# Kernel tuning notes

Hardware: AMD Instinct MI355X
Metric: run time of the kernel (lower is better)

Reference implementation:

```python
import jax, jax.numpy as jnp
import numpy as np


def _v2v_mean(X, pair_v, pair_e, num_edges):
    """Hypergraph v2v mean aggregation: vertex->edge mean, then edge->vertex mean.
    X: [N, C] vertex features; (pair_v, pair_e): incidence pairs."""
    num_v = X.shape[0]
    ones = jnp.ones((pair_v.shape[0],), X.dtype)
    # v2e mean: average member-vertex features per hyperedge
    e_sum = jax.ops.segment_sum(X[pair_v], pair_e, num_segments=num_edges)
    e_cnt = jax.ops.segment_sum(ones, pair_e, num_segments=num_edges)
    Xe = e_sum / jnp.maximum(e_cnt, 1.0)[:, None]  # [E, C]
    # e2v mean: average incident-hyperedge features per vertex
    v_sum = jax.ops.segment_sum(Xe[pair_e], pair_v, num_segments=num_v)
    v_cnt = jax.ops.segment_sum(ones, pair_v, num_segments=num_v)
    return v_sum / jnp.maximum(v_cnt, 1.0)[:, None]  # [N, C]


def setup_inputs() -> dict:
    key = jax.random.key(0)
    ks = jax.random.split(key, 6)
    N, E, P = 16384, 2048, 262144          # vertices, hyperedges, incidence pairs
    Cin, Ch, Cout = 1024, 1024, 512
    feature_hyg = jax.random.normal(ks[0], (N, Cin), jnp.float32)
    pair_v = jax.random.randint(ks[1], (P,), 0, N)
    pair_e = jax.random.randint(ks[2], (P,), 0, E)
    W1 = jax.random.normal(ks[3], (Cin, Ch), jnp.float32) / np.float32(np.sqrt(Cin))
    b1 = jnp.zeros((Ch,), jnp.float32)
    W2 = jax.random.normal(ks[4], (Ch, Cout), jnp.float32) / np.float32(np.sqrt(Ch))
    b2 = jnp.zeros((Cout,), jnp.float32)
    return {"feature_hyg": feature_hyg, "pair_v": pair_v, "pair_e": pair_e,
            "num_edges": E, "W1": W1, "b1": b1, "W2": W2, "b2": b2}


def reference(feature_hyg, pair_v, pair_e, num_edges, W1, b1, W2, b2):
    # HGNNPConv layer 1 (use_bn=False, drop_rate=0.0, eval-mode dropout)
    X = jax.nn.relu(feature_hyg @ W1 + b1)   # theta + relu
    X = _v2v_mean(X, pair_v, pair_e, num_edges)
    X = jax.nn.relu(X)                       # self.act (dropout is identity)
    # HGNNPConv layer 2 (is_last=True)
    X = jax.nn.relu(X @ W2 + b2)
    X = _v2v_mean(X, pair_v, pair_e, num_edges)
    return X
```

## Files before the change

### kernel.cpp

```cpp
#include <hip/hip_runtime.h>

typedef __attribute__((ext_vector_type(8))) short short8;
typedef __attribute__((ext_vector_type(4))) float f32x4;

constexpr int Nv   = 16384;
constexpr int Ne   = 2048;
constexpr int Np   = 262144;
constexpr int Cin  = 1024;
constexpr int Chid = 1024;
constexpr int Cout = 512;

__device__ __forceinline__ ushort f2bf(float f){
  unsigned u = __float_as_uint(f);
  u += 0x7FFFu + ((u >> 16) & 1u);
  return (ushort)(u >> 16);
}
__device__ __forceinline__ float bf2f(ushort h){
  return __uint_as_float(((unsigned)h) << 16);
}

__device__ __forceinline__ void gload16(const void* g, void* lds){
  __builtin_amdgcn_global_load_lds(
      (const __attribute__((address_space(1))) void*)g,
      (__attribute__((address_space(3))) void*)lds, 16, 0, 0);
}


__global__ void count_pairs(const int* __restrict__ pv, const int* __restrict__ pe,
                            int* __restrict__ vcnt, int* __restrict__ ecnt){
  int p = blockIdx.x * blockDim.x + threadIdx.x;
  if (p < Np){
    atomicAdd(&ecnt[pe[p]], 1);
    atomicAdd(&vcnt[pv[p]], 1);
  }
}

__global__ void scan_excl(const int* __restrict__ cnt, int* __restrict__ off, int n){
  __shared__ int wsum[16];
  __shared__ int carry_s;
  const int lane = threadIdx.x & 63, wid = threadIdx.x >> 6;
  if (threadIdx.x == 0) carry_s = 0;
  __syncthreads();
  for (int base = 0; base < n; base += 1024){
    int i = base + (int)threadIdx.x;
    int v = (i < n) ? cnt[i] : 0;
    int s = v;
#pragma unroll
    for (int d = 1; d < 64; d <<= 1){
      int t = __shfl_up(s, d, 64);
      if (lane >= d) s += t;
    }
    if (lane == 63) wsum[wid] = s;
    __syncthreads();
    int wadd = 0;
#pragma unroll
    for (int w = 0; w < 16; ++w) if (w < wid) wadd += wsum[w];
    int carry = carry_s;
    if (i < n) off[i] = carry + wadd + s - v;
    __syncthreads();
    if (threadIdx.x == 1023) carry_s = carry + wadd + s;
    __syncthreads();
  }
  if (threadIdx.x == 0) off[n] = carry_s;
}

__global__ void fill_adj(const int* __restrict__ pv, const int* __restrict__ pe,
                         const int* __restrict__ eoff, int* __restrict__ efill, int* __restrict__ eadj,
                         const int* __restrict__ voff, int* __restrict__ vfill, int* __restrict__ vadj){
  int p = blockIdx.x * blockDim.x + threadIdx.x;
  if (p < Np){
    int e = pe[p], v = pv[p];
    int ie = atomicAdd(&efill[e], 1);
    eadj[eoff[e] + ie] = v;
    int iv = atomicAdd(&vfill[v], 1);
    vadj[voff[v] + iv] = e;
  }
}


__global__ void cvt_f32_bf16(const float* __restrict__ in, ushort* __restrict__ out, int n4){
  int i = blockIdx.x * blockDim.x + threadIdx.x;
  if (i < n4){
    float4 f = ((const float4*)in)[i];
    ushort4 o;
    o.x = f2bf(f.x); o.y = f2bf(f.y); o.z = f2bf(f.z); o.w = f2bf(f.w);
    ((ushort4*)out)[i] = o;
  }
}

__global__ void transpose_cvt(const float* __restrict__ in, ushort* __restrict__ out,
                              int R, int Ccols){
  __shared__ float t[32][33];
  int c0 = blockIdx.x * 32, r0 = blockIdx.y * 32;
  int tx = threadIdx.x, ty = threadIdx.y;
  for (int j = 0; j < 32; j += 8)
    t[ty + j][tx] = in[(size_t)(r0 + ty + j) * Ccols + (c0 + tx)];
  __syncthreads();
  for (int j = 0; j < 32; j += 8)
    out[(size_t)(c0 + ty + j) * R + (r0 + tx)] = f2bf(t[tx][ty + j]);
}


template<bool BIAS_RELU, bool OUT_BF16>
__global__ __launch_bounds__(256) void gemm_bt(
    const ushort* __restrict__ A, const ushort* __restrict__ BT,
    const float* __restrict__ bias, void* __restrict__ out,
    int M, int Nn, int K)
{
  __shared__ ushort As[128 * 32];
  __shared__ ushort Bs[128 * 32];
  const int tid  = threadIdx.x;
  const int lane = tid & 63;
  const int wave = tid >> 6;
  const int wm = wave >> 1, wn = wave & 1;
  const int m0 = blockIdx.x * 128, n0 = blockIdx.y * 128;

  f32x4 acc[4][4] = {};

  const int srow = tid >> 2;
  const int scol = (tid & 3) * 8;
  ushort* ldsA0 = &As[(wave * 16) * 32];
  ushort* ldsA1 = &As[(64 + wave * 16) * 32];
  ushort* ldsB0 = &Bs[(wave * 16) * 32];
  ushort* ldsB1 = &Bs[(64 + wave * 16) * 32];

  const int fr = lane & 15;
  const int kb = (lane >> 4) * 8;

  const size_t arow0 = (size_t)(m0 + srow) * K;
  const size_t arow1 = (size_t)(m0 + 64 + srow) * K;
  const size_t brow0 = (size_t)(n0 + srow) * K;
  const size_t brow1 = (size_t)(n0 + 64 + srow) * K;

  for (int k0 = 0; k0 < K; k0 += 32){
    __syncthreads();
    gload16(A  + arow0 + k0 + scol, ldsA0);
    gload16(A  + arow1 + k0 + scol, ldsA1);
    gload16(BT + brow0 + k0 + scol, ldsB0);
    gload16(BT + brow1 + k0 + scol, ldsB1);
    __syncthreads();

    short8 af[4], bfv[4];
#pragma unroll
    for (int m = 0; m < 4; ++m) af[m]  = *(const short8*)&As[(wm * 64 + m * 16 + fr) * 32 + kb];
#pragma unroll
    for (int n = 0; n < 4; ++n) bfv[n] = *(const short8*)&Bs[(wn * 64 + n * 16 + fr) * 32 + kb];
#pragma unroll
    for (int m = 0; m < 4; ++m)
#pragma unroll
      for (int n = 0; n < 4; ++n)
        acc[m][n] = __builtin_amdgcn_mfma_f32_16x16x32_bf16(af[m], bfv[n], acc[m][n], 0, 0, 0);
  }

#pragma unroll
  for (int m = 0; m < 4; ++m){
#pragma unroll
    for (int n = 0; n < 4; ++n){
      int row0 = m0 + wm * 64 + m * 16 + ((lane >> 4) * 4);
      int col  = n0 + wn * 64 + n * 16 + (lane & 15);
      float bv = BIAS_RELU ? bias[col] : 0.0f;
#pragma unroll
      for (int i = 0; i < 4; ++i){
        int row = row0 + i;
        float v = acc[m][n][i];
        if (BIAS_RELU){ v += bv; v = v > 0.0f ? v : 0.0f; }
        if (OUT_BF16) ((ushort*)out)[(size_t)row * Nn + col] = f2bf(v);
        else          ((float*) out)[(size_t)row * Nn + col] = v;
      }
    }
  }
}


template<bool BIASRELU, bool OUTBF16>
__global__ void seg_mean512(const ushort* __restrict__ Xin, const int* __restrict__ off,
                            const int* __restrict__ adj, const float* __restrict__ bias,
                            void* __restrict__ out){
  __shared__ int idx[128];
  const int s = blockIdx.x;
  const int tid = threadIdx.x;
  const int c = tid * 4;
  const int beg = off[s], end = off[s + 1];
  float a0 = 0.f, a1 = 0.f, a2 = 0.f, a3 = 0.f;
  for (int base = beg; base < end; base += 128){
    int nch = min(128, end - base);
    __syncthreads();
    if (tid < nch) idx[tid] = adj[base + tid];
    __syncthreads();
#pragma unroll 4
    for (int j = 0; j < nch; ++j){
      const ushort4 x = *(const ushort4*)&Xin[(size_t)idx[j] * 512 + c];
      a0 += bf2f(x.x); a1 += bf2f(x.y); a2 += bf2f(x.z); a3 += bf2f(x.w);
    }
  }
  float inv = 1.0f / (float)max(end - beg, 1);
  a0 *= inv; a1 *= inv; a2 *= inv; a3 *= inv;
  if (BIASRELU){
    const float4 b = *(const float4*)&bias[c];
    a0 = fmaxf(a0 + b.x, 0.f); a1 = fmaxf(a1 + b.y, 0.f);
    a2 = fmaxf(a2 + b.z, 0.f); a3 = fmaxf(a3 + b.w, 0.f);
  }
  if (OUTBF16){
    ushort4 o = {f2bf(a0), f2bf(a1), f2bf(a2), f2bf(a3)};
    *(ushort4*)&((ushort*)out)[(size_t)s * 512 + c] = o;
  } else {
    float4 o = {a0, a1, a2, a3};
    *(float4*)&((float*)out)[(size_t)s * 512 + c] = o;
  }
}


extern "C" void kernel_launch(void* const* d_in, const int* in_sizes, int n_in,
                              void* d_out, int out_size, void* d_ws, size_t ws_size,
                              hipStream_t stream){
  (void)in_sizes; (void)n_in; (void)out_size; (void)ws_size;
  const float* feat = (const float*)d_in[0];
  const int*   pv   = (const int*)d_in[1];
  const int*   pe   = (const int*)d_in[2];
  const float* W1   = (const float*)d_in[4];
  const float* b1   = (const float*)d_in[5];
  const float* W2   = (const float*)d_in[6];
  const float* b2   = (const float*)d_in[7];

  char* ws = (char*)d_ws;
  size_t off = 0;
  auto alloc = [&](size_t bytes) -> void* {
    void* p = ws + off;
    off += (bytes + 255) & ~(size_t)255;
    return p;
  };

  char* buf0 = (char*)alloc((size_t)Nv * Cin * 2);
  ushort* Abf = (ushort*)buf0;
  ushort* Y1  = (ushort*)buf0;
  ushort* X3  = (ushort*)(buf0 + (size_t)Nv * Cout * 2);
  ushort* X1bf = (ushort*)alloc((size_t)Nv * Chid * 2);
  ushort* Ze   = (ushort*)alloc((size_t)Ne * Cout * 2);
  ushort* Xe2  = (ushort*)alloc((size_t)Ne * Cout * 2);
  ushort* W1T  = (ushort*)alloc((size_t)Chid * Cin * 2);
  ushort* W2T  = (ushort*)alloc((size_t)Cout * Chid * 2);

  int* zr     = (int*)alloc((size_t)(Ne + Nv + Ne + Nv) * 4);
  int* e_cnt  = zr;
  int* v_cnt  = zr + Ne;
  int* e_fill = zr + Ne + Nv;
  int* v_fill = zr + Ne + Nv + Ne;
  int* e_off  = (int*)alloc((size_t)(Ne + 1) * 4);
  int* v_off  = (int*)alloc((size_t)(Nv + 1) * 4);
  int* e_adj  = (int*)alloc((size_t)Np * 4);
  int* v_adj  = (int*)alloc((size_t)Np * 4);

  hipMemsetAsync(zr, 0, (size_t)(Ne + Nv + Ne + Nv) * 4, stream);
  count_pairs<<<(Np + 255) / 256, 256, 0, stream>>>(pv, pe, v_cnt, e_cnt);
  scan_excl<<<1, 1024, 0, stream>>>(e_cnt, e_off, Ne);
  scan_excl<<<1, 1024, 0, stream>>>(v_cnt, v_off, Nv);
  fill_adj<<<(Np + 255) / 256, 256, 0, stream>>>(pv, pe, e_off, e_fill, e_adj,
                                                 v_off, v_fill, v_adj);

  cvt_f32_bf16<<<(Nv * Cin / 4 + 255) / 256, 256, 0, stream>>>(feat, Abf, Nv * Cin / 4);
  transpose_cvt<<<dim3(Chid / 32, Cin / 32), dim3(32, 8), 0, stream>>>(W1, W1T, Cin, Chid);
  transpose_cvt<<<dim3(Cout / 32, Chid / 32), dim3(32, 8), 0, stream>>>(W2, W2T, Chid, Cout);

  gemm_bt<true, true><<<dim3(Nv / 128, Chid / 128), 256, 0, stream>>>(
      Abf, W1T, b1, X1bf, Nv, Chid, Cin);

  gemm_bt<false, true><<<dim3(Nv / 128, Cout / 128), 256, 0, stream>>>(
      X1bf, W2T, nullptr, Y1, Nv, Cout, Chid);

  seg_mean512<false, true><<<Ne, 128, 0, stream>>>(Y1, e_off, e_adj, nullptr, Ze);

  seg_mean512<true, true><<<Nv, 128, 0, stream>>>(Ze, v_off, v_adj, b2, X3);

  seg_mean512<false, true><<<Ne, 128, 0, stream>>>(X3, e_off, e_adj, nullptr, Xe2);
  seg_mean512<false, false><<<Nv, 128, 0, stream>>>(Xe2, v_off, v_adj, nullptr, (float*)d_out);
}
```

Measured before the change: 420.6 us.

## Double-buffer GEMM LDS tiles and split segment-mean rows across four waves

The GEMM now double-buffers its A/B LDS tiles, issuing the async global-to-LDS load for the next K-slice before running the MFMAs on the current one, with a single barrier per iteration. This is meant to hide load latency behind compute. The segment-mean kernel moves to 256 threads: each of four waves gathers a different subset of rows with 16-byte loads and two independent accumulators, then the partial sums are reduced through LDS. This raises memory-level parallelism for the gather, at the cost of extra LDS use and a reduction step.

```diff
diff --git a/kernel.cpp b/kernel.cpp
--- a/kernel.cpp
+++ b/kernel.cpp
@@ -107,8 +107,8 @@
     const float* __restrict__ bias, void* __restrict__ out,
     int M, int Nn, int K)
 {
-  __shared__ ushort As[128 * 32];
-  __shared__ ushort Bs[128 * 32];
+  __shared__ ushort As[2][128 * 32];
+  __shared__ ushort Bs[2][128 * 32];
   const int tid  = threadIdx.x;
   const int lane = tid & 63;
   const int wave = tid >> 6;
@@ -119,10 +119,8 @@
 
   const int srow = tid >> 2;
   const int scol = (tid & 3) * 8;
-  ushort* ldsA0 = &As[(wave * 16) * 32];
-  ushort* ldsA1 = &As[(64 + wave * 16) * 32];
-  ushort* ldsB0 = &Bs[(wave * 16) * 32];
-  ushort* ldsB1 = &Bs[(64 + wave * 16) * 32];
+  const int ldsbase0 = (wave * 16) * 32;
+  const int ldsbase1 = (64 + wave * 16) * 32;
 
   const int fr = lane & 15;
   const int kb = (lane >> 4) * 8;
@@ -132,24 +130,35 @@
   const size_t brow0 = (size_t)(n0 + srow) * K;
   const size_t brow1 = (size_t)(n0 + 64 + srow) * K;
 
-  for (int k0 = 0; k0 < K; k0 += 32){
-    __syncthreads();
-    gload16(A  + arow0 + k0 + scol, ldsA0);
-    gload16(A  + arow1 + k0 + scol, ldsA1);
-    gload16(BT + brow0 + k0 + scol, ldsB0);
-    gload16(BT + brow1 + k0 + scol, ldsB1);
-    __syncthreads();
+  const int nt = K >> 5;
+
+  auto stage = [&](int b, int k0){
+    gload16(A  + arow0 + k0 + scol, &As[b][ldsbase0]);
+    gload16(A  + arow1 + k0 + scol, &As[b][ldsbase1]);
+    gload16(BT + brow0 + k0 + scol, &Bs[b][ldsbase0]);
+    gload16(BT + brow1 + k0 + scol, &Bs[b][ldsbase1]);
+  };
+
+  stage(0, 0);
+  __syncthreads();
+
+  int cur = 0;
+  for (int t = 0; t < nt; ++t){
+    if (t + 1 < nt) stage(cur ^ 1, (t + 1) * 32);
 
     short8 af[4], bfv[4];
 #pragma unroll
-    for (int m = 0; m < 4; ++m) af[m]  = *(const short8*)&As[(wm * 64 + m * 16 + fr) * 32 + kb];
-#pragma unroll
-    for (int n = 0; n < 4; ++n) bfv[n] = *(const short8*)&Bs[(wn * 64 + n * 16 + fr) * 32 + kb];
+    for (int m = 0; m < 4; ++m) af[m]  = *(const short8*)&As[cur][(wm * 64 + m * 16 + fr) * 32 + kb];
+#pragma unroll
+    for (int n = 0; n < 4; ++n) bfv[n] = *(const short8*)&Bs[cur][(wn * 64 + n * 16 + fr) * 32 + kb];
 #pragma unroll
     for (int m = 0; m < 4; ++m)
 #pragma unroll
       for (int n = 0; n < 4; ++n)
         acc[m][n] = __builtin_amdgcn_mfma_f32_16x16x32_bf16(af[m], bfv[n], acc[m][n], 0, 0, 0);
+
+    __syncthreads();
+    cur ^= 1;
   }
 
 #pragma unroll
@@ -173,39 +182,63 @@
 
 
 template<bool BIASRELU, bool OUTBF16>
-__global__ void seg_mean512(const ushort* __restrict__ Xin, const int* __restrict__ off,
-                            const int* __restrict__ adj, const float* __restrict__ bias,
-                            void* __restrict__ out){
-  __shared__ int idx[128];
+__global__ __launch_bounds__(256) void seg_mean512(
+    const ushort* __restrict__ Xin, const int* __restrict__ off,
+    const int* __restrict__ adj, const float* __restrict__ bias,
+    void* __restrict__ out){
+  __shared__ int idx[256];
+  __shared__ float part[4][512];
   const int s = blockIdx.x;
-  const int tid = threadIdx.x;
-  const int c = tid * 4;
+  const int tid  = threadIdx.x;
+  const int lane = tid & 63;
+  const int wv   = tid >> 6;
+  const int c0   = lane * 8;
   const int beg = off[s], end = off[s + 1];
-  float a0 = 0.f, a1 = 0.f, a2 = 0.f, a3 = 0.f;
-  for (int base = beg; base < end; base += 128){
-    int nch = min(128, end - base);
+
+  float a0[8] = {}, a1[8] = {};
+
+  for (int base = beg; base < end; base += 256){
+    const int nch = min(256, end - base);
     __syncthreads();
     if (tid < nch) idx[tid] = adj[base + tid];
     __syncthreads();
-#pragma unroll 4
-    for (int j = 0; j < nch; ++j){
-      const ushort4 x = *(const ushort4*)&Xin[(size_t)idx[j] * 512 + c];
-      a0 += bf2f(x.x); a1 += bf2f(x.y); a2 += bf2f(x.z); a3 += bf2f(x.w);
+    int j = wv;
+    for (; j + 4 < nch; j += 8){
+      short8 x0 = *(const short8*)&Xin[(size_t)idx[j]     * 512 + c0];
+      short8 x1 = *(const short8*)&Xin[(size_t)idx[j + 4] * 512 + c0];
+#pragma unroll
+      for (int k = 0; k < 8; ++k){
+        a0[k] += bf2f((ushort)x0[k]);
+        a1[k] += bf2f((ushort)x1[k]);
+      }
     }
-  }
-  float inv = 1.0f / (float)max(end - beg, 1);
-  a0 *= inv; a1 *= inv; a2 *= inv; a3 *= inv;
+    if (j < nch){
+      short8 x0 = *(const short8*)&Xin[(size_t)idx[j] * 512 + c0];
+#pragma unroll
+      for (int k = 0; k < 8; ++k) a0[k] += bf2f((ushort)x0[k]);
+    }
+  }
+
+  f32x4 p0 = {a0[0] + a1[0], a0[1] + a1[1], a0[2] + a1[2], a0[3] + a1[3]};
+  f32x4 p1 = {a0[4] + a1[4], a0[5] + a1[5], a0[6] + a1[6], a0[7] + a1[7]};
+  *(f32x4*)&part[wv][c0]     = p0;
+  *(f32x4*)&part[wv][c0 + 4] = p1;
+  __syncthreads();
+
+  const float inv = 1.0f / (float)max(end - beg, 1);
+  const int c = tid * 2;
+  float r0 = (part[0][c]     + part[1][c]     + part[2][c]     + part[3][c])     * inv;
+  float r1 = (part[0][c + 1] + part[1][c + 1] + part[2][c + 1] + part[3][c + 1]) * inv;
   if (BIASRELU){
-    const float4 b = *(const float4*)&bias[c];
-    a0 = fmaxf(a0 + b.x, 0.f); a1 = fmaxf(a1 + b.y, 0.f);
-    a2 = fmaxf(a2 + b.z, 0.f); a3 = fmaxf(a3 + b.w, 0.f);
+    r0 = fmaxf(r0 + bias[c], 0.f);
+    r1 = fmaxf(r1 + bias[c + 1], 0.f);
   }
   if (OUTBF16){
-    ushort4 o = {f2bf(a0), f2bf(a1), f2bf(a2), f2bf(a3)};
-    *(ushort4*)&((ushort*)out)[(size_t)s * 512 + c] = o;
+    ushort2 o = {f2bf(r0), f2bf(r1)};
+    *(ushort2*)&((ushort*)out)[(size_t)s * 512 + c] = o;
   } else {
-    float4 o = {a0, a1, a2, a3};
-    *(float4*)&((float*)out)[(size_t)s * 512 + c] = o;
+    float2 o = {r0, r1};
+    *(float2*)&((float*)out)[(size_t)s * 512 + c] = o;
   }
 }
 
@@ -267,10 +300,10 @@
   gemm_bt<false, true><<<dim3(Nv / 128, Cout / 128), 256, 0, stream>>>(
       X1bf, W2T, nullptr, Y1, Nv, Cout, Chid);
 
-  seg_mean512<false, true><<<Ne, 128, 0, stream>>>(Y1, e_off, e_adj, nullptr, Ze);
-
-  seg_mean512<true, true><<<Nv, 128, 0, stream>>>(Ze, v_off, v_adj, b2, X3);
-
-  seg_mean512<false, true><<<Ne, 128, 0, stream>>>(X3, e_off, e_adj, nullptr, Xe2);
-  seg_mean512<false, false><<<Nv, 128, 0, stream>>>(Xe2, v_off, v_adj, nullptr, (float*)d_out);
-}
+  seg_mean512<false, true><<<Ne, 256, 0, stream>>>(Y1, e_off, e_adj, nullptr, Ze);
+
+  seg_mean512<true, true><<<Nv, 256, 0, stream>>>(Ze, v_off, v_adj, b2, X3);
+
+  seg_mean512<false, true><<<Ne, 256, 0, stream>>>(X3, e_off, e_adj, nullptr, Xe2);
+  seg_mean512<false, false><<<Nv, 256, 0, stream>>>(Xe2, v_off, v_adj, nullptr, (float*)d_out);
+}
```

Result: no change. 413.5 us (-1.7%).
